# Optimization experiments

Measured on AMD Instinct MI355X. Metric: run time of the kernel, lower is better.

Reference implementation:

```python
import jax, jax.numpy as jnp
import numpy as np

MS = (1, 2, 4, 8, 16, 32)  # ms_token_size; last entry == H == W
A = -0.75  # PyTorch bicubic coefficient


def _cubic_w(t, a=A):
    t = abs(float(t))
    if t <= 1.0:
        return (a + 2.0) * t**3 - (a + 3.0) * t**2 + 1.0
    if t < 2.0:
        return a * t**3 - 5.0 * a * t**2 + 8.0 * a * t - 4.0 * a
    return 0.0


def _bicubic_matrix(n_in, n_out):
    # Dense [n_out, n_in] matrix reproducing F.interpolate(mode='bicubic',
    # align_corners=False) with border-clamped taps (PyTorch semantics).
    M = np.zeros((n_out, n_in), np.float32)
    s = n_in / n_out
    for i in range(n_out):
        x = (i + 0.5) * s - 0.5
        x0 = int(np.floor(x))
        t = x - x0
        for off in (-1, 0, 1, 2):
            j = min(max(x0 + off, 0), n_in - 1)
            M[i, j] += _cubic_w(off - t)
    return jnp.asarray(M)


def _area_down(x, pn):
    # 'area' interpolation with integer factor == average pooling
    B, C, H, W = x.shape
    f = H // pn
    return x.reshape(B, C, pn, f, pn, f).mean(axis=(3, 5))


def _bicubic_up(x, Mh, Mw):
    # separable bicubic: y = Mh @ x @ Mw^T per (b, c)
    return jnp.einsum('hi,wj,bcij->bchw', Mh, Mw, x)


def setup_inputs() -> dict:
    key = jax.random.key(0)
    k1, k2 = jax.random.split(key)
    z_enc = jax.random.normal(k1, (16, 128, 32, 32), dtype=jnp.float32)
    emb = jax.random.normal(k2, (8192, 128), dtype=jnp.float32) * 1.0  # std=1.0
    return {"z_enc": z_enc, "emb": emb}


def reference(z_enc, emb):
    B, C, H, W = z_enc.shape
    n_levels = len(MS)
    # z_enc is detached in the original (z_enc.detach())
    z_rest = jax.lax.stop_gradient(z_enc)
    z_dec = jnp.zeros_like(z_rest)
    e_sq = jnp.sum(emb * emb, axis=1)  # [V]
    ret = []
    for step, pn in enumerate(MS):
        last = step == n_levels - 1
        zd = z_rest if last else _area_down(z_rest, pn)
        flat = zd.transpose(0, 2, 3, 1).reshape(-1, C)  # [B*pn*pn, C]
        # ||z||^2 + ||e||^2 - 2 z e^T
        dist = jnp.sum(flat * flat, axis=1, keepdims=True) + e_sq \
               - 2.0 * (flat @ emb.T)
        token = jnp.argmin(dist, axis=1)  # [B*pn*pn]
        zq = emb[token].reshape(B, pn, pn, C).transpose(0, 3, 1, 2)  # [B,C,pn,pn]
        if last:
            zu = zq
        else:
            Mh = _bicubic_matrix(pn, H)
            Mw = _bicubic_matrix(pn, W)
            zu = _bicubic_up(zq, Mh, Mw)
        z_dec = z_dec + zu
        z_rest = z_rest - zu
        ret.append(z_dec)
    return jnp.stack(ret)  # [n_levels, B, C, H, W]
```

## Files before the change

### kernel.cpp

```cpp
#include <hip/hip_runtime.h>
#include <hip/hip_bf16.h>

#define NCODES 8192
#define CDIM 128
#define NTOT (16*128*32*32)
#define KTOT 22272

typedef __attribute__((ext_vector_type(8))) short bf16x8;
typedef __attribute__((ext_vector_type(16))) float f32x16;
typedef unsigned long long u64;
typedef unsigned int u32;
typedef unsigned short ushort_t;

__device__ __forceinline__ ushort_t f2bf(float x) {
    u32 u = __float_as_uint(x);
    u32 r = (u + 0x7FFFu + ((u >> 16) & 1u)) >> 16;
    return (ushort_t)r;
}
__device__ __forceinline__ float bf2f(ushort_t h) {
    return __uint_as_float(((u32)h) << 16);
}

__device__ __forceinline__ void gload_lds16(const void* g, void* l) {
    __builtin_amdgcn_global_load_lds(
        (const __attribute__((address_space(1))) unsigned int*)g,
        (__attribute__((address_space(3))) unsigned int*)l, 16, 0, 0);
}

__global__ __launch_bounds__(256) void pack_emb_kernel(const float* __restrict__ src,
        ushort_t* __restrict__ dst, float* __restrict__ esq) {
    __shared__ float sm[32][129];
    int rb = blockIdx.x, t = threadIdx.x;
    int rl = t >> 3, d0 = (t & 7) * 16;
    const float4* s4 = (const float4*)(src + (size_t)(rb * 32 + rl) * CDIM + d0);
    #pragma unroll
    for (int j = 0; j < 4; j++) {
        float4 v = s4[j];
        sm[rl][d0 + 4*j + 0] = v.x; sm[rl][d0 + 4*j + 1] = v.y;
        sm[rl][d0 + 4*j + 2] = v.z; sm[rl][d0 + 4*j + 3] = v.w;
    }
    __syncthreads();
    {
        int r = t >> 3, g = t & 7;
        float s = 0.f;
        #pragma unroll
        for (int k = 0; k < 16; k++) { float x = sm[r][g * 16 + k]; s += x * x; }
        s += __shfl_xor(s, 1, 64);
        s += __shfl_xor(s, 2, 64);
        s += __shfl_xor(s, 4, 64);
        if (g == 0) esq[rb * 32 + r] = s;
    }
    #pragma unroll
    for (int k = 0; k < 2; k++) {
        int s = t + 256 * k;
        int c = s >> 6, l = s & 63;
        int r = l & 31, dbase = c * 16 + (l >> 5) * 8;
        bf16x8 vh, vl;
        #pragma unroll
        for (int e = 0; e < 8; e++) {
            float x = sm[r][dbase + e];
            ushort_t hh = f2bf(x);
            vh[e] = (short)hh;
            vl[e] = (short)f2bf(x - bf2f(hh));
        }
        size_t base = ((size_t)(rb * 8 + c) * 2) * 512 + (size_t)l * 8;
        *(bf16x8*)(dst + base)       = vh;
        *(bf16x8*)(dst + base + 512) = vl;
    }
}

__global__ __launch_bounds__(256) void down_kernel(const float* __restrict__ src,
        float* __restrict__ zd, u64* __restrict__ keys) {
    int gi = blockIdx.x * 256 + threadIdx.x;
    if (gi < KTOT) keys[gi] = ~0ull;
    int t    = gi;
    int item = t >> 6;
    int wi   = t & 63;
    int row = item >> 7, dim = item & 127;
    const float* sp = src + (((size_t)row * CDIM + dim) * 32) * 32;
    float s = 0.f;
    #pragma unroll
    for (int k = 0; k < 16; k++) {
        int flat = wi * 16 + k;
        s += sp[(flat >> 5) * 32 + (flat & 31)];
    }
    #pragma unroll
    for (int d = 32; d; d >>= 1) s += __shfl_xor(s, d, 64);
    if (wi == 0) zd[(size_t)row * CDIM + dim] = s * (1.0f / 1024.0f);
}

__global__ __launch_bounds__(512) void argmin_kernel(
        const float* __restrict__ zsrc, const ushort_t* __restrict__ bpk,
        const float* __restrict__ esq, u64* __restrict__ keys,
        int tiles, int slices, int nrows, int bchw) {
    __shared__ ushort_t lds[2][16384];
    __shared__ float es_lds[2048];

    int cps = NCODES / slices;
    int steps = cps >> 6;
    int bid = blockIdx.x;
    int tile  = bid / slices;
    int slice = bid % slices;
    int code0 = slice * cps;
    int tid = threadIdx.x, wv = tid >> 6, l = tid & 63, l31 = l & 31, lh = l >> 5;

    int rb = tile * 8 + wv;
    bf16x8 a_h[8], a_l[8];
    if (bchw) {
        int b = rb >> 5, h = rb & 31;
        const float* zr = zsrc + (size_t)b * 131072 + h * 32 + l31;
        #pragma unroll
        for (int c = 0; c < 8; c++) {
            #pragma unroll
            for (int e = 0; e < 8; e++) {
                int d = c * 16 + lh * 8 + e;
                float x = -2.0f * zr[(size_t)d * 1024];
                ushort_t hh = f2bf(x);
                a_h[c][e] = (short)hh;
                a_l[c][e] = (short)f2bf(x - bf2f(hh));
            }
        }
    } else {
        int row = rb * 32 + l31;
        if (row > nrows - 1) row = nrows - 1;
        const float* zr = zsrc + (size_t)row * CDIM + lh * 8;
        #pragma unroll
        for (int c = 0; c < 8; c++) {
            float4 f0 = *(const float4*)(zr + c * 16);
            float4 f1 = *(const float4*)(zr + c * 16 + 4);
            float xs[8] = {f0.x, f0.y, f0.z, f0.w, f1.x, f1.y, f1.z, f1.w};
            #pragma unroll
            for (int e = 0; e < 8; e++) {
                float x = -2.0f * xs[e];
                ushort_t hh = f2bf(x);
                a_h[c][e] = (short)hh;
                a_l[c][e] = (short)f2bf(x - bf2f(hh));
            }
        }
    }
    float ev0 = 0.f, ev1 = 0.f, ev2 = 0.f, ev3 = 0.f;
    if (tid < cps)        ev0 = esq[code0 + tid];
    if (512  + tid < cps) ev1 = esq[code0 + 512 + tid];
    if (1024 + tid < cps) ev2 = esq[code0 + 1024 + tid];
    if (1536 + tid < cps) ev3 = esq[code0 + 1536 + tid];
    __builtin_amdgcn_sched_barrier(0);

    const char* bbase = (const char*)bpk + (size_t)(code0 >> 6) * 32768;
    {
        const char* g0 = bbase + (size_t)wv * 4096 + (size_t)l * 16;
        ushort_t* d0 = &lds[0][wv * 2048];
        gload_lds16(g0,        d0);
        gload_lds16(g0 + 1024, d0 + 512);
        gload_lds16(g0 + 2048, d0 + 1024);
        gload_lds16(g0 + 3072, d0 + 1536);
    }
    __builtin_amdgcn_sched_barrier(0);
    if (tid < cps)        es_lds[tid] = ev0;
    if (512  + tid < cps) es_lds[512 + tid] = ev1;
    if (1024 + tid < cps) es_lds[1024 + tid] = ev2;
    if (1536 + tid < cps) es_lds[1536 + tid] = ev3;
    asm volatile("s_waitcnt lgkmcnt(0)" ::: "memory");

    float best[16];
    int   bidx[16];
    #pragma unroll
    for (int r = 0; r < 16; r++) { best[r] = 1e38f; bidx[r] = 0; }

    for (int t = 0; t < steps; ++t) {
        asm volatile("s_waitcnt vmcnt(0)" ::: "memory");
        __builtin_amdgcn_s_barrier();
        if (t + 1 < steps) {
            const char* g = bbase + (size_t)(t + 1) * 32768
                          + (size_t)wv * 4096 + (size_t)l * 16;
            ushort_t* d = &lds[(t + 1) & 1][wv * 2048];
            gload_lds16(g,        d);
            gload_lds16(g + 1024, d + 512);
            gload_lds16(g + 2048, d + 1024);
            gload_lds16(g + 3072, d + 1536);
        }
        float es0 = es_lds[(t << 6) + l31];
        float es1 = es_lds[(t << 6) + 32 + l31];
        f32x16 acc0, acc1;
        #pragma unroll
        for (int r = 0; r < 16; r++) { acc0[r] = es0; acc1[r] = es1; }
        const ushort_t* lp = &lds[t & 1][0] + l * 8;
        __builtin_amdgcn_s_setprio(1);
        #pragma unroll
        for (int c = 0; c < 8; c++) {
            bf16x8 g0h = *(const bf16x8*)(lp + (2 * c) * 512);
            bf16x8 g0l = *(const bf16x8*)(lp + (2 * c + 1) * 512);
            bf16x8 g1h = *(const bf16x8*)(lp + 8192 + (2 * c) * 512);
            bf16x8 g1l = *(const bf16x8*)(lp + 8192 + (2 * c + 1) * 512);
            acc0 = __builtin_amdgcn_mfma_f32_32x32x16_bf16(a_h[c], g0h, acc0, 0, 0, 0);
            acc1 = __builtin_amdgcn_mfma_f32_32x32x16_bf16(a_h[c], g1h, acc1, 0, 0, 0);
            acc0 = __builtin_amdgcn_mfma_f32_32x32x16_bf16(a_h[c], g0l, acc0, 0, 0, 0);
            acc1 = __builtin_amdgcn_mfma_f32_32x32x16_bf16(a_h[c], g1l, acc1, 0, 0, 0);
            acc0 = __builtin_amdgcn_mfma_f32_32x32x16_bf16(a_l[c], g0h, acc0, 0, 0, 0);
            acc1 = __builtin_amdgcn_mfma_f32_32x32x16_bf16(a_l[c], g1h, acc1, 0, 0, 0);
        }
        __builtin_amdgcn_s_setprio(0);
        int code = code0 + (t << 6) + l31;
        #pragma unroll
        for (int r = 0; r < 16; r++) {
            float s0 = acc0[r], s1 = acc1[r];
            float m  = fminf(s0, s1);
            int   ci = (s0 <= s1) ? code : code + 32;
            bool lt = m < best[r];
            best[r] = lt ? m : best[r];
            bidx[r] = lt ? ci : bidx[r];
        }
    }

    #pragma unroll
    for (int r = 0; r < 16; r++) {
        u32 fb = __float_as_uint(best[r]);
        fb = (fb & 0x80000000u) ? ~fb : (fb | 0x80000000u);
        u64 key = ((u64)fb << 32) | (u32)bidx[r];
        #pragma unroll
        for (int d = 1; d < 32; d <<= 1) {
            u64 o = __shfl_xor(key, d, 64);
            key = (o < key) ? o : key;
        }
        if (l31 == 0) {
            int rw = tile * 256 + wv * 32 + (r & 3) + 8 * (r >> 2) + 4 * lh;
            atomicMin(&keys[rw], key);
        }
    }
}

__device__ __forceinline__ float cubicw(float t) {
    float t2 = t * t;
    if (t <= 1.0f) return (1.25f * t - 2.25f) * t2 + 1.0f;
    return -0.75f * (((t - 5.0f) * t + 8.0f) * t - 4.0f);
}

__global__ __launch_bounds__(256) void up_kernel(
        const float* __restrict__ emb,
        const u64* __restrict__ keys,
        const float* __restrict__ src,
        const float* __restrict__ prev,
        float* __restrict__ zrest,
        float* __restrict__ out,
        float* __restrict__ zd_next,
        int pn, int last, int first, int pnn) {
    __shared__ float wtab[32][4];
    __shared__ int   itab[32][4];
    __shared__ float smp[512];
    int tid = threadIdx.x;
    if (!last && tid < 128) {
        int pos = tid >> 2, tap = tid & 3;
        float s  = (float)pn * (1.0f / 32.0f);
        float x  = ((float)pos + 0.5f) * s - 0.5f;
        float x0 = floorf(x);
        float t  = x - x0;
        int   off = tap - 1;
        float w  = cubicw(fabsf((float)off - t));
        int   jj = (int)x0 + off;
        jj = min(max(jj, 0), pn - 1);
        wtab[pos][tap] = w;
        itab[pos][tap] = jj;
    }
    __syncthreads();

    int t  = blockIdx.x * 256 + tid;
    int w4 = (t & 7) << 2;
    int h  = (t >> 3) & 31;
    int c  = (t >> 8) & 127;
    int b  = t >> 15;
    size_t i = (((size_t)b * CDIM + c) * 32 + h) * 32 + w4;

    float zu[4];
    if (last) {
        int kb = (b << 10) + (h << 5) + w4;
        #pragma unroll
        for (int j = 0; j < 4; j++) {
            int tok = (int)(keys[kb + j] & 0xFFFFFFFFull);
            zu[j] = emb[(size_t)tok * CDIM + c];
        }
    } else {
        int base = b * pn * pn;
        #pragma unroll
        for (int j = 0; j < 4; j++) zu[j] = 0.f;
        #pragma unroll
        for (int u = 0; u < 4; u++) {
            float whu = wtab[h][u];
            int   ih  = itab[h][u] * pn;
            #pragma unroll
            for (int j = 0; j < 4; j++) {
                float acc = 0.f;
                #pragma unroll
                for (int v = 0; v < 4; v++) {
                    int tok = (int)(keys[base + ih + itab[w4 + j][v]] & 0xFFFFFFFFull);
                    acc += wtab[w4 + j][v] * emb[(size_t)tok * CDIM + c];
                }
                zu[j] += whu * acc;
            }
        }
    }
    float4 sv = *(const float4*)(src + i);
    float4 pv = {0.f, 0.f, 0.f, 0.f};
    if (!first) pv = *(const float4*)(prev + i);
    float4 ov, rv;
    ov.x = pv.x + zu[0]; ov.y = pv.y + zu[1]; ov.z = pv.z + zu[2]; ov.w = pv.w + zu[3];
    rv.x = sv.x - zu[0]; rv.y = sv.y - zu[1]; rv.z = sv.z - zu[2]; rv.w = sv.w - zu[3];
    *(float4*)(out + i)   = ov;
    *(float4*)(zrest + i) = rv;

    if (pnn) {
        int f = 32 / pnn;
        if (f >= 4) {
            smp[h * 8 + (w4 >> 2)] = (rv.x + rv.y) + (rv.z + rv.w);
        } else {
            smp[h * 16 + (w4 >> 1)]     = rv.x + rv.y;
            smp[h * 16 + (w4 >> 1) + 1] = rv.z + rv.w;
        }
        __syncthreads();
        int W = pnn * pnn;
        if (tid < W) {
            int lb = __builtin_ctz(pnn);
            int ph = tid >> lb, pw = tid & (pnn - 1);
            float s = 0.f;
            if (f >= 4) {
                int cg = f >> 2;
                for (int u = 0; u < f; u++)
                    for (int v = 0; v < cg; v++)
                        s += smp[(ph * f + u) * 8 + pw * cg + v];
            } else {
                s = smp[(2 * ph) * 16 + pw] + smp[(2 * ph + 1) * 16 + pw];
            }
            int b2 = blockIdx.x >> 7, c2 = blockIdx.x & 127;
            int row = (b2 * pnn + ph) * pnn + pw;
            zd_next[(size_t)row * CDIM + c2] = s * (1.0f / (float)(f * f));
        }
    }
}

extern "C" void kernel_launch(void* const* d_in, const int* in_sizes, int n_in,
                              void* d_out, int out_size, void* d_ws, size_t ws_size,
                              hipStream_t stream) {
    const float* z_enc = (const float*)d_in[0];
    const float* emb   = (const float*)d_in[1];
    float* out = (float*)d_out;
    float* ws  = (float*)d_ws;

    float*    zrest  = ws;
    float*    zd_f32 = ws + 2097152;
    ushort_t* emb_pk = (ushort_t*)(ws + 4194304);
    float*    esq    = ws + 5242880;
    u64*      keys   = (u64*)(ws + 5251072);

    pack_emb_kernel<<<NCODES / 32, 256, 0, stream>>>(emb, emb_pk, esq);
    down_kernel<<<512, 256, 0, stream>>>(z_enc, zd_f32, keys);

    const int MS_[6]   = {1, 2, 4, 8, 16, 32};
    const int SL_[6]   = {128, 128, 128, 64, 16, 4};
    const int KOFF_[6] = {0, 256, 512, 768, 1792, 5888};
    for (int lvl = 0; lvl < 6; lvl++) {
        int pn     = MS_[lvl];
        int rows   = 16 * pn * pn;
        int tiles  = (rows + 255) / 256;
        int slices = SL_[lvl];
        const float* src = lvl ? zrest : z_enc;

        argmin_kernel<<<tiles * slices, 512, 0, stream>>>(
            lvl == 5 ? zrest : zd_f32, emb_pk, esq, keys + KOFF_[lvl],
            tiles, slices, rows, lvl == 5 ? 1 : 0);
        int pnn = (lvl < 4) ? MS_[lvl + 1] : 0;
        up_kernel<<<NTOT / 4 / 256, 256, 0, stream>>>(
            emb, keys + KOFF_[lvl], src, lvl ? (out + (size_t)(lvl - 1) * NTOT) : out,
            zrest, out + (size_t)lvl * NTOT, zd_f32,
            pn, lvl == 5 ? 1 : 0, lvl == 0 ? 1 : 0, pnn);
    }
}
```

Baseline: 418.3 us.

## Fuse all levels into one cooperative persistent kernel with grid syncs

Replaces the fourteen separate kernel launches (pack, down, and six argmin/upsample pairs) with a single cooperative kernel of 256 blocks that runs every stage and uses grid-wide synchronization between them. The aim is to remove launch overhead and tail gaps between the many small dependent kernels. In exchange, the upsample stage now has 256 blocks each doing four slices, and the argmin stages only use as many blocks as they had before, so some blocks idle. Grid syncs also carry their own cost, and cooperative launch limits the grid to blocks that can be co-resident.

```diff
diff --git a/kernel.cpp b/kernel.cpp
--- a/kernel.cpp
+++ b/kernel.cpp
@@ -1,5 +1,8 @@
 #include <hip/hip_runtime.h>
 #include <hip/hip_bf16.h>
+#include <hip/hip_cooperative_groups.h>
+
+namespace cg = cooperative_groups;
 
 #define NCODES 8192
 #define CDIM 128
@@ -20,318 +23,338 @@
 __device__ __forceinline__ float bf2f(ushort_t h) {
     return __uint_as_float(((u32)h) << 16);
 }
-
 __device__ __forceinline__ void gload_lds16(const void* g, void* l) {
     __builtin_amdgcn_global_load_lds(
         (const __attribute__((address_space(1))) unsigned int*)g,
         (__attribute__((address_space(3))) unsigned int*)l, 16, 0, 0);
 }
-
-__global__ __launch_bounds__(256) void pack_emb_kernel(const float* __restrict__ src,
-        ushort_t* __restrict__ dst, float* __restrict__ esq) {
-    __shared__ float sm[32][129];
-    int rb = blockIdx.x, t = threadIdx.x;
-    int rl = t >> 3, d0 = (t & 7) * 16;
-    const float4* s4 = (const float4*)(src + (size_t)(rb * 32 + rl) * CDIM + d0);
-    #pragma unroll
-    for (int j = 0; j < 4; j++) {
-        float4 v = s4[j];
-        sm[rl][d0 + 4*j + 0] = v.x; sm[rl][d0 + 4*j + 1] = v.y;
-        sm[rl][d0 + 4*j + 2] = v.z; sm[rl][d0 + 4*j + 3] = v.w;
-    }
-    __syncthreads();
-    {
-        int r = t >> 3, g = t & 7;
-        float s = 0.f;
-        #pragma unroll
-        for (int k = 0; k < 16; k++) { float x = sm[r][g * 16 + k]; s += x * x; }
-        s += __shfl_xor(s, 1, 64);
-        s += __shfl_xor(s, 2, 64);
-        s += __shfl_xor(s, 4, 64);
-        if (g == 0) esq[rb * 32 + r] = s;
-    }
-    #pragma unroll
-    for (int k = 0; k < 2; k++) {
-        int s = t + 256 * k;
-        int c = s >> 6, l = s & 63;
-        int r = l & 31, dbase = c * 16 + (l >> 5) * 8;
-        bf16x8 vh, vl;
-        #pragma unroll
-        for (int e = 0; e < 8; e++) {
-            float x = sm[r][dbase + e];
-            ushort_t hh = f2bf(x);
-            vh[e] = (short)hh;
-            vl[e] = (short)f2bf(x - bf2f(hh));
-        }
-        size_t base = ((size_t)(rb * 8 + c) * 2) * 512 + (size_t)l * 8;
-        *(bf16x8*)(dst + base)       = vh;
-        *(bf16x8*)(dst + base + 512) = vl;
-    }
-}
-
-__global__ __launch_bounds__(256) void down_kernel(const float* __restrict__ src,
-        float* __restrict__ zd, u64* __restrict__ keys) {
-    int gi = blockIdx.x * 256 + threadIdx.x;
-    if (gi < KTOT) keys[gi] = ~0ull;
-    int t    = gi;
-    int item = t >> 6;
-    int wi   = t & 63;
-    int row = item >> 7, dim = item & 127;
-    const float* sp = src + (((size_t)row * CDIM + dim) * 32) * 32;
-    float s = 0.f;
-    #pragma unroll
-    for (int k = 0; k < 16; k++) {
-        int flat = wi * 16 + k;
-        s += sp[(flat >> 5) * 32 + (flat & 31)];
-    }
-    #pragma unroll
-    for (int d = 32; d; d >>= 1) s += __shfl_xor(s, d, 64);
-    if (wi == 0) zd[(size_t)row * CDIM + dim] = s * (1.0f / 1024.0f);
-}
-
-__global__ __launch_bounds__(512) void argmin_kernel(
-        const float* __restrict__ zsrc, const ushort_t* __restrict__ bpk,
-        const float* __restrict__ esq, u64* __restrict__ keys,
-        int tiles, int slices, int nrows, int bchw) {
-    __shared__ ushort_t lds[2][16384];
-    __shared__ float es_lds[2048];
-
-    int cps = NCODES / slices;
-    int steps = cps >> 6;
-    int bid = blockIdx.x;
-    int tile  = bid / slices;
-    int slice = bid % slices;
-    int code0 = slice * cps;
-    int tid = threadIdx.x, wv = tid >> 6, l = tid & 63, l31 = l & 31, lh = l >> 5;
-
-    int rb = tile * 8 + wv;
-    bf16x8 a_h[8], a_l[8];
-    if (bchw) {
-        int b = rb >> 5, h = rb & 31;
-        const float* zr = zsrc + (size_t)b * 131072 + h * 32 + l31;
-        #pragma unroll
-        for (int c = 0; c < 8; c++) {
-            #pragma unroll
-            for (int e = 0; e < 8; e++) {
-                int d = c * 16 + lh * 8 + e;
-                float x = -2.0f * zr[(size_t)d * 1024];
-                ushort_t hh = f2bf(x);
-                a_h[c][e] = (short)hh;
-                a_l[c][e] = (short)f2bf(x - bf2f(hh));
-            }
-        }
-    } else {
-        int row = rb * 32 + l31;
-        if (row > nrows - 1) row = nrows - 1;
-        const float* zr = zsrc + (size_t)row * CDIM + lh * 8;
-        #pragma unroll
-        for (int c = 0; c < 8; c++) {
-            float4 f0 = *(const float4*)(zr + c * 16);
-            float4 f1 = *(const float4*)(zr + c * 16 + 4);
-            float xs[8] = {f0.x, f0.y, f0.z, f0.w, f1.x, f1.y, f1.z, f1.w};
-            #pragma unroll
-            for (int e = 0; e < 8; e++) {
-                float x = -2.0f * xs[e];
-                ushort_t hh = f2bf(x);
-                a_h[c][e] = (short)hh;
-                a_l[c][e] = (short)f2bf(x - bf2f(hh));
-            }
-        }
-    }
-    float ev0 = 0.f, ev1 = 0.f, ev2 = 0.f, ev3 = 0.f;
-    if (tid < cps)        ev0 = esq[code0 + tid];
-    if (512  + tid < cps) ev1 = esq[code0 + 512 + tid];
-    if (1024 + tid < cps) ev2 = esq[code0 + 1024 + tid];
-    if (1536 + tid < cps) ev3 = esq[code0 + 1536 + tid];
-    __builtin_amdgcn_sched_barrier(0);
-
-    const char* bbase = (const char*)bpk + (size_t)(code0 >> 6) * 32768;
-    {
-        const char* g0 = bbase + (size_t)wv * 4096 + (size_t)l * 16;
-        ushort_t* d0 = &lds[0][wv * 2048];
-        gload_lds16(g0,        d0);
-        gload_lds16(g0 + 1024, d0 + 512);
-        gload_lds16(g0 + 2048, d0 + 1024);
-        gload_lds16(g0 + 3072, d0 + 1536);
-    }
-    __builtin_amdgcn_sched_barrier(0);
-    if (tid < cps)        es_lds[tid] = ev0;
-    if (512  + tid < cps) es_lds[512 + tid] = ev1;
-    if (1024 + tid < cps) es_lds[1024 + tid] = ev2;
-    if (1536 + tid < cps) es_lds[1536 + tid] = ev3;
-    asm volatile("s_waitcnt lgkmcnt(0)" ::: "memory");
-
-    float best[16];
-    int   bidx[16];
-    #pragma unroll
-    for (int r = 0; r < 16; r++) { best[r] = 1e38f; bidx[r] = 0; }
-
-    for (int t = 0; t < steps; ++t) {
-        asm volatile("s_waitcnt vmcnt(0)" ::: "memory");
-        __builtin_amdgcn_s_barrier();
-        if (t + 1 < steps) {
-            const char* g = bbase + (size_t)(t + 1) * 32768
-                          + (size_t)wv * 4096 + (size_t)l * 16;
-            ushort_t* d = &lds[(t + 1) & 1][wv * 2048];
-            gload_lds16(g,        d);
-            gload_lds16(g + 1024, d + 512);
-            gload_lds16(g + 2048, d + 1024);
-            gload_lds16(g + 3072, d + 1536);
-        }
-        float es0 = es_lds[(t << 6) + l31];
-        float es1 = es_lds[(t << 6) + 32 + l31];
-        f32x16 acc0, acc1;
-        #pragma unroll
-        for (int r = 0; r < 16; r++) { acc0[r] = es0; acc1[r] = es1; }
-        const ushort_t* lp = &lds[t & 1][0] + l * 8;
-        __builtin_amdgcn_s_setprio(1);
-        #pragma unroll
-        for (int c = 0; c < 8; c++) {
-            bf16x8 g0h = *(const bf16x8*)(lp + (2 * c) * 512);
-            bf16x8 g0l = *(const bf16x8*)(lp + (2 * c + 1) * 512);
-            bf16x8 g1h = *(const bf16x8*)(lp + 8192 + (2 * c) * 512);
-            bf16x8 g1l = *(const bf16x8*)(lp + 8192 + (2 * c + 1) * 512);
-            acc0 = __builtin_amdgcn_mfma_f32_32x32x16_bf16(a_h[c], g0h, acc0, 0, 0, 0);
-            acc1 = __builtin_amdgcn_mfma_f32_32x32x16_bf16(a_h[c], g1h, acc1, 0, 0, 0);
-            acc0 = __builtin_amdgcn_mfma_f32_32x32x16_bf16(a_h[c], g0l, acc0, 0, 0, 0);
-            acc1 = __builtin_amdgcn_mfma_f32_32x32x16_bf16(a_h[c], g1l, acc1, 0, 0, 0);
-            acc0 = __builtin_amdgcn_mfma_f32_32x32x16_bf16(a_l[c], g0h, acc0, 0, 0, 0);
-            acc1 = __builtin_amdgcn_mfma_f32_32x32x16_bf16(a_l[c], g1h, acc1, 0, 0, 0);
-        }
-        __builtin_amdgcn_s_setprio(0);
-        int code = code0 + (t << 6) + l31;
-        #pragma unroll
-        for (int r = 0; r < 16; r++) {
-            float s0 = acc0[r], s1 = acc1[r];
-            float m  = fminf(s0, s1);
-            int   ci = (s0 <= s1) ? code : code + 32;
-            bool lt = m < best[r];
-            best[r] = lt ? m : best[r];
-            bidx[r] = lt ? ci : bidx[r];
-        }
-    }
-
-    #pragma unroll
-    for (int r = 0; r < 16; r++) {
-        u32 fb = __float_as_uint(best[r]);
-        fb = (fb & 0x80000000u) ? ~fb : (fb | 0x80000000u);
-        u64 key = ((u64)fb << 32) | (u32)bidx[r];
-        #pragma unroll
-        for (int d = 1; d < 32; d <<= 1) {
-            u64 o = __shfl_xor(key, d, 64);
-            key = (o < key) ? o : key;
-        }
-        if (l31 == 0) {
-            int rw = tile * 256 + wv * 32 + (r & 3) + 8 * (r >> 2) + 4 * lh;
-            atomicMin(&keys[rw], key);
-        }
-    }
-}
-
 __device__ __forceinline__ float cubicw(float t) {
     float t2 = t * t;
     if (t <= 1.0f) return (1.25f * t - 2.25f) * t2 + 1.0f;
     return -0.75f * (((t - 5.0f) * t + 8.0f) * t - 4.0f);
 }
 
-__global__ __launch_bounds__(256) void up_kernel(
-        const float* __restrict__ emb,
-        const u64* __restrict__ keys,
-        const float* __restrict__ src,
-        const float* __restrict__ prev,
-        float* __restrict__ zrest,
-        float* __restrict__ out,
-        float* __restrict__ zd_next,
-        int pn, int last, int first, int pnn) {
-    __shared__ float wtab[32][4];
-    __shared__ int   itab[32][4];
-    __shared__ float smp[512];
-    int tid = threadIdx.x;
-    if (!last && tid < 128) {
-        int pos = tid >> 2, tap = tid & 3;
-        float s  = (float)pn * (1.0f / 32.0f);
-        float x  = ((float)pos + 0.5f) * s - 0.5f;
-        float x0 = floorf(x);
-        float t  = x - x0;
-        int   off = tap - 1;
-        float w  = cubicw(fabsf((float)off - t));
-        int   jj = (int)x0 + off;
-        jj = min(max(jj, 0), pn - 1);
-        wtab[pos][tap] = w;
-        itab[pos][tap] = jj;
-    }
-    __syncthreads();
-
-    int t  = blockIdx.x * 256 + tid;
-    int w4 = (t & 7) << 2;
-    int h  = (t >> 3) & 31;
-    int c  = (t >> 8) & 127;
-    int b  = t >> 15;
-    size_t i = (((size_t)b * CDIM + c) * 32 + h) * 32 + w4;
-
-    float zu[4];
-    if (last) {
-        int kb = (b << 10) + (h << 5) + w4;
-        #pragma unroll
-        for (int j = 0; j < 4; j++) {
-            int tok = (int)(keys[kb + j] & 0xFFFFFFFFull);
-            zu[j] = emb[(size_t)tok * CDIM + c];
+__global__ __launch_bounds__(512) void mega_kernel(
+        const float* __restrict__ z_enc, const float* __restrict__ emb,
+        float* __restrict__ out, float* __restrict__ zrest,
+        float* __restrict__ zd, ushort_t* __restrict__ emb_pk,
+        float* __restrict__ esq, u64* __restrict__ keys_all) {
+    cg::grid_group grid = cg::this_grid();
+    __shared__ __align__(16) char smem[73728];
+    int bid = blockIdx.x, tid = threadIdx.x;
+    int wv = tid >> 6, l = tid & 63, l31 = l & 31, lh = l >> 5;
+
+    {
+        float (*sm)[129] = (float(*)[129])smem;
+        if (tid < 256) {
+            int t = tid, rl = t >> 3, d0 = (t & 7) * 16;
+            const float4* s4 = (const float4*)(emb + (size_t)(bid * 32 + rl) * CDIM + d0);
+            #pragma unroll
+            for (int j = 0; j < 4; j++) {
+                float4 v = s4[j];
+                sm[rl][d0 + 4*j + 0] = v.x; sm[rl][d0 + 4*j + 1] = v.y;
+                sm[rl][d0 + 4*j + 2] = v.z; sm[rl][d0 + 4*j + 3] = v.w;
+            }
+        } else {
+            int gi = bid * 256 + (tid - 256);
+            if (gi < KTOT) keys_all[gi] = ~0ull;
+            int item = gi >> 5, wi = gi & 31;
+            int row = item >> 7, dim = item & 127;
+            const float* sp = z_enc + (((size_t)row * CDIM + dim) * 32) * 32;
+            float s = 0.f;
+            #pragma unroll
+            for (int k = 0; k < 32; k++) {
+                int flat = wi * 32 + k;
+                s += sp[(flat >> 5) * 32 + (flat & 31)];
+            }
+            #pragma unroll
+            for (int d = 16; d; d >>= 1) s += __shfl_xor(s, d, 64);
+            if (wi == 0) zd[(size_t)row * CDIM + dim] = s * (1.0f / 1024.0f);
         }
-    } else {
-        int base = b * pn * pn;
-        #pragma unroll
-        for (int j = 0; j < 4; j++) zu[j] = 0.f;
-        #pragma unroll
-        for (int u = 0; u < 4; u++) {
-            float whu = wtab[h][u];
-            int   ih  = itab[h][u] * pn;
-            #pragma unroll
-            for (int j = 0; j < 4; j++) {
-                float acc = 0.f;
-                #pragma unroll
-                for (int v = 0; v < 4; v++) {
-                    int tok = (int)(keys[base + ih + itab[w4 + j][v]] & 0xFFFFFFFFull);
-                    acc += wtab[w4 + j][v] * emb[(size_t)tok * CDIM + c];
-                }
-                zu[j] += whu * acc;
+        __syncthreads();
+        if (tid < 256) {
+            int t = tid;
+            {
+                int r = t >> 3, g = t & 7;
+                float s = 0.f;
+                #pragma unroll
+                for (int k = 0; k < 16; k++) { float x = sm[r][g * 16 + k]; s += x * x; }
+                s += __shfl_xor(s, 1, 64);
+                s += __shfl_xor(s, 2, 64);
+                s += __shfl_xor(s, 4, 64);
+                if (g == 0) esq[bid * 32 + r] = s;
+            }
+            #pragma unroll
+            for (int k = 0; k < 2; k++) {
+                int s = t + 256 * k;
+                int c = s >> 6, ll = s & 63;
+                int r = ll & 31, dbase = c * 16 + (ll >> 5) * 8;
+                bf16x8 vh, vl;
+                #pragma unroll
+                for (int e = 0; e < 8; e++) {
+                    float x = sm[r][dbase + e];
+                    ushort_t hh = f2bf(x);
+                    vh[e] = (short)hh;
+                    vl[e] = (short)f2bf(x - bf2f(hh));
+                }
+                size_t base = ((size_t)(bid * 8 + c) * 2) * 512 + (size_t)ll * 8;
+                *(bf16x8*)(emb_pk + base)       = vh;
+                *(bf16x8*)(emb_pk + base + 512) = vl;
             }
         }
     }
-    float4 sv = *(const float4*)(src + i);
-    float4 pv = {0.f, 0.f, 0.f, 0.f};
-    if (!first) pv = *(const float4*)(prev + i);
-    float4 ov, rv;
-    ov.x = pv.x + zu[0]; ov.y = pv.y + zu[1]; ov.z = pv.z + zu[2]; ov.w = pv.w + zu[3];
-    rv.x = sv.x - zu[0]; rv.y = sv.y - zu[1]; rv.z = sv.z - zu[2]; rv.w = sv.w - zu[3];
-    *(float4*)(out + i)   = ov;
-    *(float4*)(zrest + i) = rv;
-
-    if (pnn) {
-        int f = 32 / pnn;
-        if (f >= 4) {
-            smp[h * 8 + (w4 >> 2)] = (rv.x + rv.y) + (rv.z + rv.w);
-        } else {
-            smp[h * 16 + (w4 >> 1)]     = rv.x + rv.y;
-            smp[h * 16 + (w4 >> 1) + 1] = rv.z + rv.w;
+    __threadfence();
+    grid.sync();
+
+    const int MS_[6]   = {1, 2, 4, 8, 16, 32};
+    const int TIL_[6]  = {1, 1, 1, 4, 16, 64};
+    const int SLC_[6]  = {128, 128, 128, 64, 16, 4};
+    const int KOFF_[6] = {0, 256, 512, 768, 1792, 5888};
+
+    for (int lvl = 0; lvl < 6; lvl++) {
+        int pn = MS_[lvl];
+        int rows = 16 * pn * pn;
+        int tiles = TIL_[lvl], slices = SLC_[lvl];
+        u64* keys = keys_all + KOFF_[lvl];
+
+        if (bid < tiles * slices) {
+            ushort_t* ldsA = (ushort_t*)smem;
+            float* es_lds  = (float*)(smem + 65536);
+            int cps = NCODES / slices;
+            int steps = cps >> 6;
+            int tile = bid / slices, slice = bid % slices;
+            int code0 = slice * cps;
+
+            int rb = tile * 8 + wv;
+            bf16x8 a_h[8], a_l[8];
+            if (lvl == 5) {
+                int b = rb >> 5, h = rb & 31;
+                const float* zr = zrest + (size_t)b * 131072 + h * 32 + l31;
+                #pragma unroll
+                for (int c = 0; c < 8; c++) {
+                    #pragma unroll
+                    for (int e = 0; e < 8; e++) {
+                        int d = c * 16 + lh * 8 + e;
+                        float x = -2.0f * zr[(size_t)d * 1024];
+                        ushort_t hh = f2bf(x);
+                        a_h[c][e] = (short)hh;
+                        a_l[c][e] = (short)f2bf(x - bf2f(hh));
+                    }
+                }
+            } else {
+                int row = rb * 32 + l31;
+                if (row > rows - 1) row = rows - 1;
+                const float* zr = zd + (size_t)row * CDIM + lh * 8;
+                #pragma unroll
+                for (int c = 0; c < 8; c++) {
+                    float4 f0 = *(const float4*)(zr + c * 16);
+                    float4 f1 = *(const float4*)(zr + c * 16 + 4);
+                    float xs[8] = {f0.x, f0.y, f0.z, f0.w, f1.x, f1.y, f1.z, f1.w};
+                    #pragma unroll
+                    for (int e = 0; e < 8; e++) {
+                        float x = -2.0f * xs[e];
+                        ushort_t hh = f2bf(x);
+                        a_h[c][e] = (short)hh;
+                        a_l[c][e] = (short)f2bf(x - bf2f(hh));
+                    }
+                }
+            }
+            float ev0 = 0.f, ev1 = 0.f, ev2 = 0.f, ev3 = 0.f;
+            if (tid < cps)        ev0 = esq[code0 + tid];
+            if (512  + tid < cps) ev1 = esq[code0 + 512 + tid];
+            if (1024 + tid < cps) ev2 = esq[code0 + 1024 + tid];
+            if (1536 + tid < cps) ev3 = esq[code0 + 1536 + tid];
+            __builtin_amdgcn_sched_barrier(0);
+
+            const char* bbase = (const char*)emb_pk + (size_t)(code0 >> 6) * 32768;
+            {
+                const char* g0 = bbase + (size_t)wv * 4096 + (size_t)l * 16;
+                ushort_t* d0 = &ldsA[wv * 2048];
+                gload_lds16(g0,        d0);
+                gload_lds16(g0 + 1024, d0 + 512);
+                gload_lds16(g0 + 2048, d0 + 1024);
+                gload_lds16(g0 + 3072, d0 + 1536);
+            }
+            __builtin_amdgcn_sched_barrier(0);
+            if (tid < cps)        es_lds[tid] = ev0;
+            if (512  + tid < cps) es_lds[512 + tid] = ev1;
+            if (1024 + tid < cps) es_lds[1024 + tid] = ev2;
+            if (1536 + tid < cps) es_lds[1536 + tid] = ev3;
+            asm volatile("s_waitcnt lgkmcnt(0)" ::: "memory");
+
+            float best[16];
+            int   bidx[16];
+            #pragma unroll
+            for (int r = 0; r < 16; r++) { best[r] = 1e38f; bidx[r] = 0; }
+
+            for (int t = 0; t < steps; ++t) {
+                asm volatile("s_waitcnt vmcnt(0)" ::: "memory");
+                __builtin_amdgcn_s_barrier();
+                if (t + 1 < steps) {
+                    const char* g = bbase + (size_t)(t + 1) * 32768
+                                  + (size_t)wv * 4096 + (size_t)l * 16;
+                    ushort_t* d = &ldsA[((t + 1) & 1) * 16384 + wv * 2048];
+                    gload_lds16(g,        d);
+                    gload_lds16(g + 1024, d + 512);
+                    gload_lds16(g + 2048, d + 1024);
+                    gload_lds16(g + 3072, d + 1536);
+                }
+                float es0 = es_lds[(t << 6) + l31];
+                float es1 = es_lds[(t << 6) + 32 + l31];
+                f32x16 acc0, acc1;
+                #pragma unroll
+                for (int r = 0; r < 16; r++) { acc0[r] = es0; acc1[r] = es1; }
+                const ushort_t* lp = &ldsA[(t & 1) * 16384] + l * 8;
+                __builtin_amdgcn_s_setprio(1);
+                #pragma unroll
+                for (int c = 0; c < 8; c++) {
+                    bf16x8 g0h = *(const bf16x8*)(lp + (2 * c) * 512);
+                    bf16x8 g0l = *(const bf16x8*)(lp + (2 * c + 1) * 512);
+                    bf16x8 g1h = *(const bf16x8*)(lp + 8192 + (2 * c) * 512);
+                    bf16x8 g1l = *(const bf16x8*)(lp + 8192 + (2 * c + 1) * 512);
+                    acc0 = __builtin_amdgcn_mfma_f32_32x32x16_bf16(a_h[c], g0h, acc0, 0, 0, 0);
+                    acc1 = __builtin_amdgcn_mfma_f32_32x32x16_bf16(a_h[c], g1h, acc1, 0, 0, 0);
+                    acc0 = __builtin_amdgcn_mfma_f32_32x32x16_bf16(a_h[c], g0l, acc0, 0, 0, 0);
+                    acc1 = __builtin_amdgcn_mfma_f32_32x32x16_bf16(a_h[c], g1l, acc1, 0, 0, 0);
+                    acc0 = __builtin_amdgcn_mfma_f32_32x32x16_bf16(a_l[c], g0h, acc0, 0, 0, 0);
+                    acc1 = __builtin_amdgcn_mfma_f32_32x32x16_bf16(a_l[c], g1h, acc1, 0, 0, 0);
+                }
+                __builtin_amdgcn_s_setprio(0);
+                int code = code0 + (t << 6) + l31;
+                #pragma unroll
+                for (int r = 0; r < 16; r++) {
+                    float s0 = acc0[r], s1 = acc1[r];
+                    float m  = fminf(s0, s1);
+                    int   ci = (s0 <= s1) ? code : code + 32;
+                    bool lt = m < best[r];
+                    best[r] = lt ? m : best[r];
+                    bidx[r] = lt ? ci : bidx[r];
+                }
+            }
+
+            #pragma unroll
+            for (int r = 0; r < 16; r++) {
+                u32 fb = __float_as_uint(best[r]);
+                fb = (fb & 0x80000000u) ? ~fb : (fb | 0x80000000u);
+                u64 key = ((u64)fb << 32) | (u32)bidx[r];
+                #pragma unroll
+                for (int d = 1; d < 32; d <<= 1) {
+                    u64 o = __shfl_xor(key, d, 64);
+                    key = (o < key) ? o : key;
+                }
+                if (l31 == 0) {
+                    int rw = tile * 256 + wv * 32 + (r & 3) + 8 * (r >> 2) + 4 * lh;
+                    atomicMin(&keys[rw], key);
+                }
+            }
         }
-        __syncthreads();
-        int W = pnn * pnn;
-        if (tid < W) {
-            int lb = __builtin_ctz(pnn);
-            int ph = tid >> lb, pw = tid & (pnn - 1);
-            float s = 0.f;
-            if (f >= 4) {
-                int cg = f >> 2;
-                for (int u = 0; u < f; u++)
-                    for (int v = 0; v < cg; v++)
-                        s += smp[(ph * f + u) * 8 + pw * cg + v];
-            } else {
-                s = smp[(2 * ph) * 16 + pw] + smp[(2 * ph + 1) * 16 + pw];
-            }
-            int b2 = blockIdx.x >> 7, c2 = blockIdx.x & 127;
-            int row = (b2 * pnn + ph) * pnn + pw;
-            zd_next[(size_t)row * CDIM + c2] = s * (1.0f / (float)(f * f));
+        __threadfence();
+        grid.sync();
+
+        {
+            int last = (lvl == 5), first = (lvl == 0);
+            int pnn = (lvl < 4) ? MS_[lvl + 1] : 0;
+            float (*wtab)[4] = (float(*)[4])smem;
+            int   (*itab)[4] = (int(*)[4])(smem + 512);
+            float* smpb      = (float*)(smem + 1024);
+            if (!last && tid < 128) {
+                int pos = tid >> 2, tap = tid & 3;
+                float s  = (float)pn * (1.0f / 32.0f);
+                float x  = ((float)pos + 0.5f) * s - 0.5f;
+                float x0 = floorf(x);
+                float tt = x - x0;
+                int   off = tap - 1;
+                float w  = cubicw(fabsf((float)off - tt));
+                int   jj = (int)x0 + off;
+                jj = min(max(jj, 0), pn - 1);
+                wtab[pos][tap] = w;
+                itab[pos][tap] = jj;
+            }
+            __syncthreads();
+
+            const float* srcp = lvl ? zrest : z_enc;
+            const float* prevp = out + (size_t)(lvl ? (lvl - 1) : 0) * NTOT;
+            float* outp = out + (size_t)lvl * NTOT;
+            int t256 = tid & 255;
+            int half = tid >> 8;
+            int w4 = (t256 & 7) << 2;
+            int h  = t256 >> 3;
+            float* smpp = smpb + half * 512;
+
+            for (int it = 0; it < 4; it++) {
+                int p = bid * 8 + it * 2 + half;
+                int b = p >> 7, c = p & 127;
+                size_t i = (((size_t)b * CDIM + c) * 32 + h) * 32 + w4;
+
+                float zu[4];
+                if (last) {
+                    int kb = (b << 10) + (h << 5) + w4;
+                    #pragma unroll
+                    for (int j = 0; j < 4; j++) {
+                        int tok = (int)(keys[kb + j] & 0xFFFFFFFFull);
+                        zu[j] = emb[(size_t)tok * CDIM + c];
+                    }
+                } else {
+                    int base = b * pn * pn;
+                    #pragma unroll
+                    for (int j = 0; j < 4; j++) zu[j] = 0.f;
+                    #pragma unroll
+                    for (int u = 0; u < 4; u++) {
+                        float whu = wtab[h][u];
+                        int   ih  = itab[h][u] * pn;
+                        #pragma unroll
+                        for (int j = 0; j < 4; j++) {
+                            float acc = 0.f;
+                            #pragma unroll
+                            for (int v = 0; v < 4; v++) {
+                                int tok = (int)(keys[base + ih + itab[w4 + j][v]] & 0xFFFFFFFFull);
+                                acc += wtab[w4 + j][v] * emb[(size_t)tok * CDIM + c];
+                            }
+                            zu[j] += whu * acc;
+                        }
+                    }
+                }
+                float4 sv = *(const float4*)(srcp + i);
+                float4 pv = {0.f, 0.f, 0.f, 0.f};
+                if (!first) pv = *(const float4*)(prevp + i);
+                float4 ov, rv;
+                ov.x = pv.x + zu[0]; ov.y = pv.y + zu[1];
+                ov.z = pv.z + zu[2]; ov.w = pv.w + zu[3];
+                rv.x = sv.x - zu[0]; rv.y = sv.y - zu[1];
+                rv.z = sv.z - zu[2]; rv.w = sv.w - zu[3];
+                *(float4*)(outp + i)  = ov;
+                *(float4*)(zrest + i) = rv;
+
+                if (pnn) {
+                    int f = 32 / pnn;
+                    if (f >= 4) {
+                        smpp[h * 8 + (w4 >> 2)] = (rv.x + rv.y) + (rv.z + rv.w);
+                    } else {
+                        smpp[h * 16 + (w4 >> 1)]     = rv.x + rv.y;
+                        smpp[h * 16 + (w4 >> 1) + 1] = rv.z + rv.w;
+                    }
+                    __syncthreads();
+                    int W = pnn * pnn;
+                    if (t256 < W) {
+                        int lb = __builtin_ctz(pnn);
+                        int ph = t256 >> lb, pw = t256 & (pnn - 1);
+                        float s = 0.f;
+                        if (f >= 4) {
+                            int cg2 = f >> 2;
+                            for (int u = 0; u < f; u++)
+                                for (int v = 0; v < cg2; v++)
+                                    s += smpp[(ph * f + u) * 8 + pw * cg2 + v];
+                        } else {
+                            s = smpp[(2 * ph) * 16 + pw] + smpp[(2 * ph + 1) * 16 + pw];
+                        }
+                        int row = (b * pnn + ph) * pnn + pw;
+                        zd[(size_t)row * CDIM + c] = s * (1.0f / (float)(f * f));
+                    }
+                    __syncthreads();
+                }
+            }
         }
+        if (lvl < 5) { __threadfence(); grid.sync(); }
     }
 }
 
@@ -349,26 +372,8 @@
     float*    esq    = ws + 5242880;
     u64*      keys   = (u64*)(ws + 5251072);
 
-    pack_emb_kernel<<<NCODES / 32, 256, 0, stream>>>(emb, emb_pk, esq);
-    down_kernel<<<512, 256, 0, stream>>>(z_enc, zd_f32, keys);
-
-    const int MS_[6]   = {1, 2, 4, 8, 16, 32};
-    const int SL_[6]   = {128, 128, 128, 64, 16, 4};
-    const int KOFF_[6] = {0, 256, 512, 768, 1792, 5888};
-    for (int lvl = 0; lvl < 6; lvl++) {
-        int pn     = MS_[lvl];
-        int rows   = 16 * pn * pn;
-        int tiles  = (rows + 255) / 256;
-        int slices = SL_[lvl];
-        const float* src = lvl ? zrest : z_enc;
-
-        argmin_kernel<<<tiles * slices, 512, 0, stream>>>(
-            lvl == 5 ? zrest : zd_f32, emb_pk, esq, keys + KOFF_[lvl],
-            tiles, slices, rows, lvl == 5 ? 1 : 0);
-        int pnn = (lvl < 4) ? MS_[lvl + 1] : 0;
-        up_kernel<<<NTOT / 4 / 256, 256, 0, stream>>>(
-            emb, keys + KOFF_[lvl], src, lvl ? (out + (size_t)(lvl - 1) * NTOT) : out,
-            zrest, out + (size_t)lvl * NTOT, zd_f32,
-            pn, lvl == 5 ? 1 : 0, lvl == 0 ? 1 : 0, pnn);
-    }
-}
+    void* args[] = {(void*)&z_enc, (void*)&emb, (void*)&out, (void*)&zrest,
+                    (void*)&zd_f32, (void*)&emb_pk, (void*)&esq, (void*)&keys};
+    hipLaunchCooperativeKernel((void*)mega_kernel, dim3(256), dim3(512),
+                               args, 0, stream);
+}
```

Result: slower. 1.161 ms (+177.7%).
